# Kernel tuning notes

Hardware: AMD Instinct MI355X
Metric: run time of the kernel (lower is better)

The kernel has to match this reference:

```python
import jax, jax.numpy as jnp
import numpy as np

EPS = 1e-12  # F.normalize eps


def setup_inputs() -> dict:
    key = jax.random.key(0)
    ks = jax.random.split(key, 3)
    B, C, D, R = 4096, 32, 128, 8
    return {
        "source": jax.random.normal(ks[0], (B, C, D), dtype=jnp.float32),
        "data": jax.random.normal(ks[1], (B, C, D), dtype=jnp.float32),
        "W": jax.random.normal(ks[2], (R, D, D), dtype=jnp.float32) * (1.0 / np.sqrt(D)),
        "a": jnp.ones((R, C, D), dtype=jnp.float32),
        "c": jnp.ones((R, C, D), dtype=jnp.float32),
        "d": jnp.zeros((R, C, D), dtype=jnp.float32),
    }


def reference(source, data, W, a, c, d):
    # Generate all reflection directions in one batched GEMM:
    # Linear(bias=False): x @ W_r^T, W_r is [out, in]
    v = jnp.einsum("bci,roi->rbco", source, W)          # [R, B, C, D]
    # DynamicTanh: tanh(a*x)*c + d, params [R, C, D] broadcast over batch
    v = jnp.tanh(a[:, None] * v) * c[:, None] + d[:, None]
    # F.normalize(p=2, dim=-1) with eps clamp
    norm = jnp.linalg.norm(v, axis=-1, keepdims=True)
    v = v / jnp.maximum(norm, EPS)

    # Sequential Householder reflections H_R(...H_2(H_1(x)))
    def step(x, vec):
        dot = jnp.sum(vec * x, axis=-1, keepdims=True)  # [B, C, 1]
        return x - 2.0 * vec * dot, None

    out, _ = jax.lax.scan(step, data, v)
    return out
```

## Files before the change

kernel.cpp:

```cpp
#include <hip/hip_runtime.h>
#include <stdint.h>

#define B_DIM 4096
#define C_DIM 32
#define D_DIM 128
#define R_DIM 8
#define BM    64
#define NTHREADS 256

typedef __bf16 bf16x8 __attribute__((ext_vector_type(8)));
typedef float  f32x4  __attribute__((ext_vector_type(4)));

__device__ __forceinline__ uint32_t f2bf(float f) {
  uint32_t u = __float_as_uint(f);
  return (u + 0x7FFFu + ((u >> 16) & 1u)) >> 16;
}

#if __has_builtin(__builtin_amdgcn_exp2f)
#define EXP2F(x) __builtin_amdgcn_exp2f(x)
#else
#define EXP2F(x) exp2f(x)
#endif
#if __has_builtin(__builtin_amdgcn_rcpf)
#define RCPF(x) __builtin_amdgcn_rcpf(x)
#else
#define RCPF(x) (1.0f / (x))
#endif

__device__ __forceinline__ void load_lds16(const void* g, void* l) {
  __builtin_amdgcn_global_load_lds(
      (const __attribute__((address_space(1))) uint32_t*)g,
      (__attribute__((address_space(3))) uint32_t*)l, 16, 0, 0);
}

template <int CTRL>
__device__ __forceinline__ float ror_add(float v) {
  int r = __builtin_amdgcn_update_dpp(0, __builtin_bit_cast(int, v), CTRL, 0xf, 0xf, true);
  return v + __builtin_bit_cast(float, r);
}
__device__ __forceinline__ float red16(float v) {
  v = ror_add<0x128>(v);
  v = ror_add<0x124>(v);
  v = ror_add<0x122>(v);
  v = ror_add<0x121>(v);
  return v;
}

__global__ void prep_w(const float* __restrict__ W, uint32_t* __restrict__ ws) {
  uint32_t t = blockIdx.x * 256u + threadIdx.x;
  uint32_t c  = t >> 2;
  uint32_t j  = t & 3u;
  uint32_t ln = c & 63u;
  uint32_t kt = (c >> 6) & 3u;
  uint32_t n  = (c >> 8) & 7u;
  uint32_t r  = c >> 11;
  uint32_t o  = n * 16u + (ln & 15u);
  uint32_t k  = kt * 32u + (ln >> 4) * 8u + j * 2u;
  const float2 w2 = *reinterpret_cast<const float2*>(
      W + ((size_t)(r * 128u + o)) * 128u + k);
  ws[t] = f2bf(w2.x) | (f2bf(w2.y) << 16);
}

__global__ void prep_acd(const float* __restrict__ A, const float* __restrict__ C,
                         const float* __restrict__ D, float* __restrict__ oA,
                         float2* __restrict__ oMC) {
  uint32_t t = blockIdx.x * 256u + threadIdx.x;
  uint32_t col = t & 127u, r = (t >> 7) & 7u, c = t >> 10;
  uint32_t in = (r * 32u + c) * 128u + col;
  float av = A[in], cv = C[in], dv = D[in];
  uint32_t idx = (c * 8u + r) * 128u + col;
  oA[idx]  = av * 2.88539008177793f;
  oMC[idx] = make_float2(-2.f * cv, cv + dv);
}

__global__ __launch_bounds__(NTHREADS, 3)
void rot_kernel(const float* __restrict__ src, const float* __restrict__ data,
                const uint8_t* __restrict__ wsw, const uint8_t* __restrict__ wsA,
                const uint8_t* __restrict__ wsMC, float* __restrict__ out)
{
  __shared__ __align__(16) unsigned char ldsW[32768];
  __shared__ __align__(16) float  ldsA[8 * 128];
  __shared__ __align__(16) float2 ldsMC[8 * 128];

  const uint32_t tid  = threadIdx.x;
  const uint32_t lane = tid & 63u;
  const uint32_t wid  = tid >> 6;
  const uint32_t l15  = lane & 15u;
  const uint32_t lg   = lane >> 4;

  const uint32_t c0   = blockIdx.x & 31u;
  const uint32_t rowb = (blockIdx.x >> 5) * BM + wid * 16u;

  #pragma unroll
  for (int j = 0; j < 8; ++j)
    load_lds16(wsw + wid * 1024u + (uint32_t)j * 4096u + lane * 16u,
               &ldsW[wid * 1024u + (uint32_t)j * 4096u]);
  load_lds16(wsA + (uint32_t)c0 * 4096u + wid * 1024u + lane * 16u,
             (uint8_t*)ldsA + wid * 1024u);
  #pragma unroll
  for (int j = 0; j < 2; ++j)
    load_lds16(wsMC + (uint32_t)c0 * 8192u + wid * 1024u + (uint32_t)j * 4096u + lane * 16u,
               (uint8_t*)ldsMC + wid * 1024u + (uint32_t)j * 4096u);

  f32x4 x[8];
  #pragma unroll
  for (int q = 0; q < 4; ++q) {
    const float* xr = data + ((size_t)(rowb + lg * 4 + q) * C_DIM + c0) * D_DIM;
    #pragma unroll
    for (int n = 0; n < 8; ++n) x[n][q] = xr[n * 16 + l15];
  }

  bf16x8 af[4];
  {
    const float* sr = src + ((size_t)(rowb + l15) * C_DIM + c0) * D_DIM + lg * 8u;
    #pragma unroll
    for (int kt = 0; kt < 4; ++kt) {
      float4 f0 = *reinterpret_cast<const float4*>(sr + kt * 32);
      float4 f1 = *reinterpret_cast<const float4*>(sr + kt * 32 + 4);
      union { uint32_t u[4]; bf16x8 v; } p;
      p.u[0] = f2bf(f0.x) | (f2bf(f0.y) << 16);
      p.u[1] = f2bf(f0.z) | (f2bf(f0.w) << 16);
      p.u[2] = f2bf(f1.x) | (f2bf(f1.y) << 16);
      p.u[3] = f2bf(f1.z) | (f2bf(f1.w) << 16);
      af[kt] = p.v;
    }
  }

  __syncthreads();

  for (int r = 0; r < R_DIM; ++r) {
    const uint32_t rb = lane * 16u;
    f32x4 acc[8];
    #pragma unroll
    for (int n = 0; n < 8; ++n) acc[n] = (f32x4){0.f, 0.f, 0.f, 0.f};
    #pragma unroll
    for (int kt = 0; kt < 4; ++kt) {
      #pragma unroll
      for (int nh = 0; nh < 8; nh += 4) {
        bf16x8 bq[4];
        #pragma unroll
        for (int i = 0; i < 4; ++i)
          bq[i] = *reinterpret_cast<const bf16x8*>(
              &ldsW[rb + (uint32_t)(((nh + i) * 4 + kt) * 1024)]);
        #pragma unroll
        for (int i = 0; i < 4; ++i)
          acc[nh + i] = __builtin_amdgcn_mfma_f32_16x16x32_bf16(af[kt], bq[i], acc[nh + i], 0, 0, 0);
      }
    }

    __syncthreads();

    if (r < 7) {
      const uint8_t* g = wsw + (uint32_t)(r + 1) * 32768u;
      #pragma unroll
      for (int j = 0; j < 8; ++j)
        load_lds16(g + wid * 1024u + (uint32_t)j * 4096u + lane * 16u,
                   &ldsW[wid * 1024u + (uint32_t)j * 4096u]);
    }

    f32x4 s2 = {0.f,0.f,0.f,0.f}, tx = {0.f,0.f,0.f,0.f};
    #pragma unroll
    for (int n = 0; n < 8; ++n) {
      float  a2 = ldsA [r * 128 + n * 16 + l15];
      float2 mc = ldsMC[r * 128 + n * 16 + l15];
      f32x4 z = acc[n] * a2;
      f32x4 ep;
      #pragma unroll
      for (int q = 0; q < 4; ++q) ep[q] = EXP2F(z[q]);
      ep = ep + 1.0f;
      f32x4 pr;
      #pragma unroll
      for (int q = 0; q < 4; ++q) pr[q] = RCPF(ep[q]);
      f32x4 t = pr * mc.x + mc.y;
      acc[n] = t;
      s2 = s2 + t * t;
      tx = tx + t * x[n];
    }
    f32x4 sc;
    #pragma unroll
    for (int q = 0; q < 4; ++q) {
      float s = red16(s2[q]);
      float d = red16(tx[q]);
      sc[q] = -2.f * d * RCPF(fmaxf(s, 1e-24f));
    }
    #pragma unroll
    for (int n = 0; n < 8; ++n)
      x[n] = x[n] + sc * acc[n];

    __syncthreads();
  }

  #pragma unroll
  for (int q = 0; q < 4; ++q) {
    float* orow = out + ((size_t)(rowb + lg * 4 + q) * C_DIM + c0) * D_DIM;
    #pragma unroll
    for (int n = 0; n < 8; ++n) orow[n * 16 + l15] = x[n][q];
  }
}

extern "C" void kernel_launch(void* const* d_in, const int* in_sizes, int n_in,
                              void* d_out, int out_size, void* d_ws, size_t ws_size,
                              hipStream_t stream) {
  const float* src  = (const float*)d_in[0];
  const float* data = (const float*)d_in[1];
  const float* W    = (const float*)d_in[2];
  const float* Aa   = (const float*)d_in[3];
  const float* Cc   = (const float*)d_in[4];
  const float* Dd   = (const float*)d_in[5];
  float* out = (float*)d_out;

  uint8_t* wsW  = (uint8_t*)d_ws;
  uint8_t* wsA  = wsW + 262144;
  uint8_t* wsMC = wsA + 131072;

  prep_w<<<dim3(256), dim3(256), 0, stream>>>(W, (uint32_t*)wsW);
  prep_acd<<<dim3(128), dim3(256), 0, stream>>>(Aa, Cc, Dd, (float*)wsA, (float2*)wsMC);

  dim3 grid((B_DIM / BM) * C_DIM);
  dim3 block(NTHREADS);
  rot_kernel<<<grid, block, 0, stream>>>(src, data, wsW, wsA, wsMC, out);
}
```

Before: 85.08 us.

## Double-buffer W in LDS and software-pipeline epilogue with next GEMM

Doubles the LDS buffer for W so the next reflection's weights load asynchronously while the current one is used, which removes one barrier per iteration. The loop is fully unrolled with ping-pong accumulators so that the tanh, normalize and Householder work for step r-1 interleaves with the MFMAs of step r, hiding the transcendental and reduction latency behind matrix work. The cost is a larger LDS footprint (64KB for W) and higher register pressure from two accumulator sets, so launch bounds drop from 3 to 2 blocks per SM, which reduces occupancy.

```diff
diff --git a/kernel.cpp b/kernel.cpp
--- a/kernel.cpp
+++ b/kernel.cpp
@@ -73,12 +73,82 @@
   oMC[idx] = make_float2(-2.f * cv, cv + dv);
 }
 
-__global__ __launch_bounds__(NTHREADS, 3)
+template <int R>
+__device__ __forceinline__ void iter_body(
+    const uint8_t* __restrict__ wsw, unsigned char* ldsW,
+    const float* ldsA, const float2* ldsMC,
+    uint32_t lane, uint32_t wid, uint32_t l15,
+    const bf16x8 (&af)[4], f32x4 (&x)[8],
+    f32x4 (&accCur)[8], f32x4 (&accPrev)[8])
+{
+  if constexpr (R < 7) {
+    const uint8_t* g = wsw + (uint32_t)(R + 1) * 32768u;
+    unsigned char* lb = ldsW + (uint32_t)(((R + 1) & 1) * 32768);
+    #pragma unroll
+    for (int j = 0; j < 8; ++j)
+      load_lds16(g + wid * 1024u + (uint32_t)j * 4096u + lane * 16u,
+                 lb + wid * 1024u + (uint32_t)j * 4096u);
+  }
+
+  const unsigned char* bufR = ldsW + (uint32_t)((R & 1) * 32768) + lane * 16u;
+  #pragma unroll
+  for (int n = 0; n < 8; ++n) accCur[n] = (f32x4){0.f, 0.f, 0.f, 0.f};
+
+  f32x4 s2 = {0.f, 0.f, 0.f, 0.f}, tx = {0.f, 0.f, 0.f, 0.f};
+  #pragma unroll
+  for (int kt = 0; kt < 4; ++kt) {
+    bf16x8 bq[8];
+    #pragma unroll
+    for (int n = 0; n < 8; ++n)
+      bq[n] = *reinterpret_cast<const bf16x8*>(
+          bufR + (uint32_t)((n * 4 + kt) * 1024));
+    #pragma unroll
+    for (int n = 0; n < 8; ++n)
+      accCur[n] = __builtin_amdgcn_mfma_f32_16x16x32_bf16(af[kt], bq[n], accCur[n], 0, 0, 0);
+
+    if constexpr (R >= 1) {
+      #pragma unroll
+      for (int nn = 0; nn < 2; ++nn) {
+        const int n = kt * 2 + nn;
+        float  a2 = ldsA [(R - 1) * 128 + n * 16 + l15];
+        float2 mc = ldsMC[(R - 1) * 128 + n * 16 + l15];
+        f32x4 z = accPrev[n] * a2;
+        f32x4 ep;
+        #pragma unroll
+        for (int q = 0; q < 4; ++q) ep[q] = EXP2F(z[q]);
+        ep = ep + 1.0f;
+        f32x4 pr;
+        #pragma unroll
+        for (int q = 0; q < 4; ++q) pr[q] = RCPF(ep[q]);
+        f32x4 t = pr * mc.x + mc.y;
+        accPrev[n] = t;
+        s2 = s2 + t * t;
+        tx = tx + t * x[n];
+      }
+    }
+  }
+  if constexpr (R >= 1) {
+    f32x4 sc;
+    #pragma unroll
+    for (int q = 0; q < 4; ++q) {
+      float s = red16(s2[q]);
+      float d = red16(tx[q]);
+      sc[q] = -2.f * d * RCPF(fmaxf(s, 1e-24f));
+    }
+    #pragma unroll
+    for (int n = 0; n < 8; ++n)
+      x[n] = x[n] + sc * accPrev[n];
+  }
+
+  __syncthreads();
+}
+
+__global__ __launch_bounds__(NTHREADS, 2)
 void rot_kernel(const float* __restrict__ src, const float* __restrict__ data,
                 const uint8_t* __restrict__ wsw, const uint8_t* __restrict__ wsA,
                 const uint8_t* __restrict__ wsMC, float* __restrict__ out)
 {
-  __shared__ __align__(16) unsigned char ldsW[32768];
+  __shared__ __align__(16) unsigned char ldsW[2 * 32768];
   __shared__ __align__(16) float  ldsA[8 * 128];
   __shared__ __align__(16) float2 ldsMC[8 * 128];
 
@@ -128,42 +198,23 @@
 
   __syncthreads();
 
-  for (int r = 0; r < R_DIM; ++r) {
-    const uint32_t rb = lane * 16u;
-    f32x4 acc[8];
-    #pragma unroll
-    for (int n = 0; n < 8; ++n) acc[n] = (f32x4){0.f, 0.f, 0.f, 0.f};
-    #pragma unroll
-    for (int kt = 0; kt < 4; ++kt) {
-      #pragma unroll
-      for (int nh = 0; nh < 8; nh += 4) {
-        bf16x8 bq[4];
-        #pragma unroll
-        for (int i = 0; i < 4; ++i)
-          bq[i] = *reinterpret_cast<const bf16x8*>(
-              &ldsW[rb + (uint32_t)(((nh + i) * 4 + kt) * 1024)]);
-        #pragma unroll
-        for (int i = 0; i < 4; ++i)
-          acc[nh + i] = __builtin_amdgcn_mfma_f32_16x16x32_bf16(af[kt], bq[i], acc[nh + i], 0, 0, 0);
-      }
-    }
-
-    __syncthreads();
-
-    if (r < 7) {
-      const uint8_t* g = wsw + (uint32_t)(r + 1) * 32768u;
-      #pragma unroll
-      for (int j = 0; j < 8; ++j)
-        load_lds16(g + wid * 1024u + (uint32_t)j * 4096u + lane * 16u,
-                   &ldsW[wid * 1024u + (uint32_t)j * 4096u]);
-    }
-
+  f32x4 accA[8], accB[8];
+  iter_body<0>(wsw, ldsW, ldsA, ldsMC, lane, wid, l15, af, x, accA, accB);
+  iter_body<1>(wsw, ldsW, ldsA, ldsMC, lane, wid, l15, af, x, accB, accA);
+  iter_body<2>(wsw, ldsW, ldsA, ldsMC, lane, wid, l15, af, x, accA, accB);
+  iter_body<3>(wsw, ldsW, ldsA, ldsMC, lane, wid, l15, af, x, accB, accA);
+  iter_body<4>(wsw, ldsW, ldsA, ldsMC, lane, wid, l15, af, x, accA, accB);
+  iter_body<5>(wsw, ldsW, ldsA, ldsMC, lane, wid, l15, af, x, accB, accA);
+  iter_body<6>(wsw, ldsW, ldsA, ldsMC, lane, wid, l15, af, x, accA, accB);
+  iter_body<7>(wsw, ldsW, ldsA, ldsMC, lane, wid, l15, af, x, accB, accA);
+
+  {
     f32x4 s2 = {0.f,0.f,0.f,0.f}, tx = {0.f,0.f,0.f,0.f};
     #pragma unroll
     for (int n = 0; n < 8; ++n) {
-      float  a2 = ldsA [r * 128 + n * 16 + l15];
-      float2 mc = ldsMC[r * 128 + n * 16 + l15];
-      f32x4 z = acc[n] * a2;
+      float  a2 = ldsA [7 * 128 + n * 16 + l15];
+      float2 mc = ldsMC[7 * 128 + n * 16 + l15];
+      f32x4 z = accB[n] * a2;
       f32x4 ep;
       #pragma unroll
       for (int q = 0; q < 4; ++q) ep[q] = EXP2F(z[q]);
@@ -172,7 +223,7 @@
       #pragma unroll
       for (int q = 0; q < 4; ++q) pr[q] = RCPF(ep[q]);
       f32x4 t = pr * mc.x + mc.y;
-      acc[n] = t;
+      accB[n] = t;
       s2 = s2 + t * t;
       tx = tx + t * x[n];
     }
@@ -185,9 +236,7 @@
     }
     #pragma unroll
     for (int n = 0; n < 8; ++n)
-      x[n] = x[n] + sc * acc[n];
-
-    __syncthreads();
+      x[n] = x[n] + sc * accB[n];
   }
 
   #pragma unroll
```

New measurement: 95.11 us (median of 2 runs). +11.8%, slower.
